# Kernel tuning notes

Measured on AMD Instinct MI355X. Metric: run time of the kernel, lower is better.

## Reference

```python
import jax, jax.numpy as jnp
import numpy as np

B, S, E, H = 2, 2048, 1024, 16
D = E // H  # head_dim = 64


def _rope(x):
    # x: (B, H, S, D); torchtune-style interleaved rotary embedding
    s, d = x.shape[-2], x.shape[-1]
    inv_freq = 1.0 / (10000.0 ** (jnp.arange(0, d, 2, dtype=jnp.float32) / d))  # (d/2,)
    freqs = jnp.arange(s, dtype=jnp.float32)[:, None] * inv_freq[None, :]       # (S, d/2)
    cos, sin = jnp.cos(freqs), jnp.sin(freqs)
    x1, x2 = x[..., 0::2], x[..., 1::2]
    o1 = x1 * cos - x2 * sin
    o2 = x2 * cos + x1 * sin
    return jnp.stack([o1, o2], axis=-1).reshape(x.shape)


def setup_inputs() -> dict:
    key = jax.random.key(0)
    kx, kq, kk, kv, ko = jax.random.split(key, 5)
    std = 1.0 / np.sqrt(E)
    return {
        "x": jax.random.normal(kx, (B, S, E), dtype=jnp.float32),
        "W_q": jax.random.normal(kq, (E, E), dtype=jnp.float32) * std,
        "W_k": jax.random.normal(kk, (E, E), dtype=jnp.float32) * std,
        "W_v": jax.random.normal(kv, (E, E), dtype=jnp.float32) * std,
        "W_o": jax.random.normal(ko, (E, E), dtype=jnp.float32) * std,
    }


def reference(x, W_q, W_k, W_v, W_o):
    b, s, e = x.shape
    h, d = H, e // H
    # nn.Linear: y = x @ W.T  (weights are (out, in))
    q = (x @ W_q.T).reshape(b, s, h, d).transpose(0, 2, 1, 3)  # (B,H,S,D)
    k = (x @ W_k.T).reshape(b, s, h, d).transpose(0, 2, 1, 3)
    v = (x @ W_v.T).reshape(b, s, h, d).transpose(0, 2, 1, 3)
    q = _rope(q)
    k = _rope(k)
    attn_scale = 1.0 / np.sqrt(e)  # NOTE: scales by sqrt(hidden_dim), as in source
    scores = jnp.einsum("bhsd,bhtd->bhst", q, k) * attn_scale  # (B,H,S,S)
    causal = jnp.triu(jnp.ones((s, s), dtype=bool), k=1)
    scores = jnp.where(causal, -jnp.inf, scores)
    probs = jax.nn.softmax(scores, axis=-1)  # dropout is identity in eval
    out = jnp.einsum("bhst,bhtd->bhsd", probs, v)
    out = out.transpose(0, 2, 1, 3).reshape(b, s, e)
    return out @ W_o.T
```

## Files before the change

### kernel.cpp

```cpp
#include <hip/hip_runtime.h>
#include <hip/hip_bf16.h>

#define BATCH 2
#define SEQ   2048
#define EMB   1024
#define NH    16
#define HD    64
#define MROWS (BATCH*SEQ)
#define NX    (MROWS*EMB)
#define NW    (EMB*EMB)

using f32x4  = __attribute__((ext_vector_type(4))) float;
using bf16x8 = __attribute__((ext_vector_type(8))) short;

#define GLOBAL_AS(p) ((const __attribute__((address_space(1))) void*)(p))
#define LDS_AS(p)    ((__attribute__((address_space(3))) void*)(p))

#define ROPE_L2 0.4152410118609203f
#define QSCALE  0.045084220027780106f

__global__ void fused_cast_kernel(const float* __restrict__ x,
                                  const float* __restrict__ Wq,
                                  const float* __restrict__ Wk,
                                  const float* __restrict__ Wv,
                                  const float* __restrict__ Wo,
                                  __hip_bfloat16* __restrict__ xb,
                                  __hip_bfloat16* __restrict__ Wqkvb,
                                  __hip_bfloat16* __restrict__ Wob,
                                  float2* __restrict__ ctab) {
    if (blockIdx.x >= 4096) {
        int e  = (blockIdx.x - 4096) * 256 + threadIdx.x;
        int s  = e >> 5;
        int ip = e & 31;
        float inv = exp2f(-(float)ip * ROPE_L2);
        float fr  = (float)s * inv;
        float2 cs;
        cs.x = cosf(fr);
        cs.y = sinf(fr);
        ctab[e] = cs;
        return;
    }
    size_t i8 = (size_t)(blockIdx.x * 256 + threadIdx.x) * 8;
    const float* src;
    __hip_bfloat16* dst;
    if (i8 < (size_t)NX) {
        src = x + i8;
        dst = xb + i8;
    } else {
        size_t w = i8 - NX;
        int which = (int)(w >> 20);
        size_t local = w & (NW - 1);
        if (which < 3) {
            src = (which == 0 ? Wq : (which == 1 ? Wk : Wv)) + local;
            dst = Wqkvb + w;
        } else {
            src = Wo + local;
            dst = Wob + local;
        }
    }
    float4 a = *(const float4*)(src);
    float4 b = *(const float4*)(src + 4);
    union { uint4 u; ushort s[8]; } o;
    const float* f = (const float*)&a;
#pragma unroll
    for (int j = 0; j < 4; ++j) {
        __hip_bfloat16 h = __float2bfloat16(f[j]);
        o.s[j] = *(ushort*)&h;
    }
    f = (const float*)&b;
#pragma unroll
    for (int j = 0; j < 4; ++j) {
        __hip_bfloat16 h = __float2bfloat16(f[j]);
        o.s[4 + j] = *(ushort*)&h;
    }
    *(uint4*)dst = o.u;
}

__global__ __launch_bounds__(256) void gemm_qkv_kernel(
        const __hip_bfloat16* __restrict__ A,
        const __hip_bfloat16* __restrict__ W,
        __hip_bfloat16* __restrict__ Qo,
        __hip_bfloat16* __restrict__ Ko,
        __hip_bfloat16* __restrict__ Vo,
        const float2* __restrict__ ctab, int M, int K) {
    __shared__ __hip_bfloat16 As[128 * 64];
    __shared__ __hip_bfloat16 Bs[128 * 64];

    const int tid  = threadIdx.x;
    const int wave = tid >> 6;
    const int lane = tid & 63;
    const int quad = lane >> 4;
    const int l16  = lane & 15;
    const int m0   = blockIdx.y * 128;
    const int n0   = blockIdx.x * 128;
    const int wm   = (wave >> 1) * 64;
    const int wn   = (wave & 1) * 64;
    const int xr   = l16 & 7;

    f32x4 acc[4][4] = {};

    for (int k0 = 0; k0 < K; k0 += 64) {
#pragma unroll
        for (int it = 0; it < 4; ++it) {
            int flat = (wave * 4 + it) * 64 + lane;
            int row  = flat >> 3;
            int g    = (flat & 7) ^ (row & 7);
            const __hip_bfloat16* ga = A + (size_t)(m0 + row) * K + k0 + g * 8;
            const __hip_bfloat16* gb = W + (size_t)(n0 + row) * K + k0 + g * 8;
            __builtin_amdgcn_global_load_lds(GLOBAL_AS(ga),
                LDS_AS(As + (size_t)(wave * 4 + it) * 512), 16, 0, 0);
            __builtin_amdgcn_global_load_lds(GLOBAL_AS(gb),
                LDS_AS(Bs + (size_t)(wave * 4 + it) * 512), 16, 0, 0);
        }
        __syncthreads();

#pragma unroll
        for (int kk = 0; kk < 2; ++kk) {
            const int kg = (kk * 4 + quad) ^ xr;
            bf16x8 af[4], bfr[4];
#pragma unroll
            for (int i = 0; i < 4; ++i) {
                af[i]  = *(const bf16x8*)(&As[(wm + i * 16 + l16) * 64 + kg * 8]);
                bfr[i] = *(const bf16x8*)(&Bs[(wn + i * 16 + l16) * 64 + kg * 8]);
            }
#pragma unroll
            for (int i = 0; i < 4; ++i)
#pragma unroll
                for (int j = 0; j < 4; ++j)
                    acc[i][j] = __builtin_amdgcn_mfma_f32_16x16x32_bf16(
                        af[i], bfr[j], acc[i][j], 0, 0, 0);
        }
        __syncthreads();
    }

    const int tens = n0 >> 10;
    __hip_bfloat16* outp = (tens == 0) ? Qo : ((tens == 1) ? Ko : Vo);
    const int nbase = n0 & 1023;
    if (tens < 2) {
        const float sgn   = (l16 & 1) ? 1.0f : -1.0f;
        const float qmul  = (tens == 0) ? QSCALE : 1.0f;
#pragma unroll
        for (int i = 0; i < 4; ++i)
#pragma unroll
            for (int j = 0; j < 4; ++j) {
                int col  = nbase + wn + j * 16 + l16;
                int ip   = ((wn + j * 16 + l16) & 63) >> 1;
                int row0 = m0 + wm + i * 16 + quad * 4;
#pragma unroll
                for (int rr = 0; rr < 4; ++rr) {
                    float v = acc[i][j][rr];
                    float p = __shfl_xor(v, 1);
                    int sp  = (row0 + rr) & (SEQ - 1);
                    float2 cs = ctab[sp * 32 + ip];
                    float o = (v * cs.x + sgn * p * cs.y) * qmul;
                    outp[(size_t)(row0 + rr) * EMB + col] = __float2bfloat16(o);
                }
            }
    } else {
#pragma unroll
        for (int i = 0; i < 4; ++i)
#pragma unroll
            for (int j = 0; j < 4; ++j) {
                int col  = nbase + wn + j * 16 + l16;
                int row0 = m0 + wm + i * 16 + quad * 4;
#pragma unroll
                for (int rr = 0; rr < 4; ++rr)
                    outp[(size_t)(row0 + rr) * EMB + col] = __float2bfloat16(acc[i][j][rr]);
            }
    }
}

__global__ __launch_bounds__(256) void gemm_oproj_kernel(
        const __hip_bfloat16* __restrict__ A,
        const __hip_bfloat16* __restrict__ Bm,
        float* __restrict__ C, int M, int N, int K) {
    __shared__ __hip_bfloat16 As[128 * 64];
    __shared__ __hip_bfloat16 Bs[64 * 64];

    const int tid  = threadIdx.x;
    const int wave = tid >> 6;
    const int lane = tid & 63;
    const int quad = lane >> 4;
    const int l16  = lane & 15;
    const int m0   = blockIdx.y * 128;
    const int n0   = blockIdx.x * 64;
    const int wm   = (wave >> 1) * 64;
    const int wn   = (wave & 1) * 32;
    const int xr   = l16 & 7;

    f32x4 acc[4][2] = {};

    for (int k0 = 0; k0 < K; k0 += 64) {
#pragma unroll
        for (int it = 0; it < 4; ++it) {
            int flat = (wave * 4 + it) * 64 + lane;
            int row  = flat >> 3;
            int g    = (flat & 7) ^ (row & 7);
            const __hip_bfloat16* ga = A + (size_t)(m0 + row) * K + k0 + g * 8;
            __builtin_amdgcn_global_load_lds(GLOBAL_AS(ga),
                LDS_AS(As + (size_t)(wave * 4 + it) * 512), 16, 0, 0);
        }
#pragma unroll
        for (int it = 0; it < 2; ++it) {
            int flat = (wave * 2 + it) * 64 + lane;
            int row  = flat >> 3;
            int g    = (flat & 7) ^ (row & 7);
            const __hip_bfloat16* gb = Bm + (size_t)(n0 + row) * K + k0 + g * 8;
            __builtin_amdgcn_global_load_lds(GLOBAL_AS(gb),
                LDS_AS(Bs + (size_t)(wave * 2 + it) * 512), 16, 0, 0);
        }
        __syncthreads();

#pragma unroll
        for (int kk = 0; kk < 2; ++kk) {
            const int kg = (kk * 4 + quad) ^ xr;
            bf16x8 af[4], bfr[2];
#pragma unroll
            for (int i = 0; i < 4; ++i)
                af[i] = *(const bf16x8*)(&As[(wm + i * 16 + l16) * 64 + kg * 8]);
#pragma unroll
            for (int j = 0; j < 2; ++j)
                bfr[j] = *(const bf16x8*)(&Bs[(wn + j * 16 + l16) * 64 + kg * 8]);
#pragma unroll
            for (int i = 0; i < 4; ++i)
#pragma unroll
                for (int j = 0; j < 2; ++j)
                    acc[i][j] = __builtin_amdgcn_mfma_f32_16x16x32_bf16(
                        af[i], bfr[j], acc[i][j], 0, 0, 0);
        }
        __syncthreads();
    }

#pragma unroll
    for (int i = 0; i < 4; ++i)
#pragma unroll
        for (int j = 0; j < 2; ++j) {
            int col  = n0 + wn + j * 16 + l16;
            int row0 = m0 + wm + i * 16 + quad * 4;
#pragma unroll
            for (int rr = 0; rr < 4; ++rr)
                C[(size_t)(row0 + rr) * N + col] = acc[i][j][rr];
        }
}

__device__ inline uint pack_bf16(float a, float b) {
    __hip_bfloat16 ha = __float2bfloat16(a), hb = __float2bfloat16(b);
    return (uint)*(ushort*)&ha | ((uint)*(ushort*)&hb << 16);
}

__global__ __launch_bounds__(256) void attn_mfma_kernel(
        const __hip_bfloat16* __restrict__ Qb,
        const __hip_bfloat16* __restrict__ Kb,
        const __hip_bfloat16* __restrict__ Vb,
        __hip_bfloat16* __restrict__ Attnb,
        __hip_bfloat16* __restrict__ Opart,
        float* __restrict__ Lpart) {
    const int bx   = blockIdx.x;
    const int bh   = blockIdx.y;
    const int b    = bh >> 4;
    const int h    = bh & (NH - 1);
    const int tid  = threadIdx.x;
    const int wave = tid >> 6;
    const int lane = tid & 63;
    const int quad = lane >> 4;
    const int l16  = lane & 15;

    __shared__ __hip_bfloat16 Ks[2][64 * 64];
    __shared__ uint VTs[2][64][33];

    const int vtp = tid >> 3;
    const int sg  = tid & 7;
    const int lr  = lane >> 3;
    const int lg  = (lane & 7) ^ lr;
    const size_t ksrc_lane = (size_t)lr * EMB + lg * 8;

    const __hip_bfloat16* Kbase = Kb + (size_t)b * SEQ * EMB + h * HD;
    const __hip_bfloat16* Vbase = Vb + (size_t)b * SEQ * EMB + h * HD;

    union { uint u[4]; bf16x8 v; } onesu;
    onesu.u[0] = 0x3F803F80u; onesu.u[1] = 0x3F803F80u;
    onesu.u[2] = 0x3F803F80u; onesu.u[3] = 0x3F803F80u;
    const bf16x8 ones = onesu.v;

    const bool isA = (bx < 16);
    const int p   = isA ? bx : bx - 16;
    const int q0  = 31 - p;
    const int k00 = isA ? 0 : 17;
    const int n0s = isA ? 17 : (15 - p);
    const int q1  = p;
    const int n1s = isA ? 0 : (p + 1);

    for (int s = 0; s < 2; ++s) {
        const int qt = s ? q1 : q0;
        const int k0 = s ? 0 : k00;
        const int nt = s ? n1s : n0s;
        if (nt <= 0) continue;
        const bool finalSeg = (!isA && s == 1);
        const int wrow = qt * 64 + wave * 16;

        __syncthreads();

        bf16x8 qf[2];
        {
            const __hip_bfloat16* qp =
                Qb + (size_t)(b * SEQ + wrow + l16) * EMB + h * HD + quad * 8;
            qf[0] = *(const bf16x8*)(qp);
            qf[1] = *(const bf16x8*)(qp + 32);
        }

        f32x4 of[4]  = {};
        f32x4 of_sum = {};

        const __hip_bfloat16* kgp = Kbase + (size_t)k0 * 64 * EMB;
        const __hip_bfloat16* vgp = Vbase + (size_t)(k0 * 64 + 2 * vtp) * EMB + sg * 8;
        uint4 vr0 = *(const uint4*)(vgp);
        uint4 vr1 = *(const uint4*)(vgp + EMB);
#pragma unroll
        for (int it = 0; it < 2; ++it)
            __builtin_amdgcn_global_load_lds(
                GLOBAL_AS(kgp + (size_t)(wave * 2 + it) * 8 * EMB + ksrc_lane),
                LDS_AS(&Ks[0][(wave * 2 + it) * 512]), 16, 0, 0);

        for (int i = 0; i < nt; ++i) {
            const int cur = i & 1;
            const int kt  = k0 + i;

            {
                const uint* v0u = (const uint*)&vr0;
                const uint* v1u = (const uint*)&vr1;
#pragma unroll
                for (int j = 0; j < 4; ++j) {
                    VTs[cur][sg * 8 + 2 * j][vtp] =
                        __builtin_amdgcn_perm(v1u[j], v0u[j], 0x05040100u);
                    VTs[cur][sg * 8 + 2 * j + 1][vtp] =
                        __builtin_amdgcn_perm(v1u[j], v0u[j], 0x07060302u);
                }
            }
            __syncthreads();

            if (i + 1 < nt) {
                kgp += (size_t)64 * EMB;
                vgp += (size_t)64 * EMB;
                vr0 = *(const uint4*)(vgp);
                vr1 = *(const uint4*)(vgp + EMB);
#pragma unroll
                for (int it = 0; it < 2; ++it)
                    __builtin_amdgcn_global_load_lds(
                        GLOBAL_AS(kgp + (size_t)(wave * 2 + it) * 8 * EMB + ksrc_lane),
                        LDS_AS(&Ks[cur ^ 1][(wave * 2 + it) * 512]), 16, 0, 0);
            }

            const bool diag = (kt == qt);
            const __hip_bfloat16* KsC = Ks[cur];
            f32x4 sc[4];
            __builtin_amdgcn_s_setprio(1);
#pragma unroll
            for (int mb = 0; mb < 4; ++mb) {
                f32x4 a = {};
                if (!(diag && mb > wave)) {
                    int krow = mb * 16 + l16;
#pragma unroll
                    for (int kb = 0; kb < 2; ++kb) {
                        int kg = (kb * 4 + quad) ^ (krow & 7);
                        bf16x8 kf = *(const bf16x8*)(&KsC[krow * 64 + kg * 8]);
                        a = __builtin_amdgcn_mfma_f32_16x16x32_bf16(kf, qf[kb], a, 0, 0, 0);
                    }
                }
                sc[mb] = a;
            }
            __builtin_amdgcn_s_setprio(0);

            if (diag) {
#pragma unroll
                for (int mb = 0; mb < 4; ++mb)
#pragma unroll
                    for (int r = 0; r < 4; ++r)
                        if (mb * 16 + quad * 4 + r > wave * 16 + l16)
                            sc[mb][r] = -16384.0f;
            }

#pragma unroll
            for (int mb = 0; mb < 4; ++mb)
#pragma unroll
                for (int r = 0; r < 4; ++r)
                    sc[mb][r] = exp2f(sc[mb][r]);

            bf16x8 pf[2];
            {
                union { uint u[4]; bf16x8 v; } t;
                t.u[0] = pack_bf16(sc[0][0], sc[0][1]);
                t.u[1] = pack_bf16(sc[0][2], sc[0][3]);
                t.u[2] = pack_bf16(sc[1][0], sc[1][1]);
                t.u[3] = pack_bf16(sc[1][2], sc[1][3]);
                pf[0] = t.v;
                t.u[0] = pack_bf16(sc[2][0], sc[2][1]);
                t.u[1] = pack_bf16(sc[2][2], sc[2][3]);
                t.u[2] = pack_bf16(sc[3][0], sc[3][1]);
                t.u[3] = pack_bf16(sc[3][2], sc[3][3]);
                pf[1] = t.v;
            }

            const uint* VT0 = &VTs[cur][0][0];
            __builtin_amdgcn_s_setprio(1);
#pragma unroll
            for (int nb = 0; nb < 4; ++nb) {
                const uint* vrow = VT0 + (size_t)(nb * 16 + l16) * 33;
#pragma unroll
                for (int c = 0; c < 2; ++c) {
                    union { uint u[4]; bf16x8 v; } vf;
                    vf.u[0] = vrow[c * 16 + 2 * quad];
                    vf.u[1] = vrow[c * 16 + 2 * quad + 1];
                    vf.u[2] = vrow[c * 16 + 8 + 2 * quad];
                    vf.u[3] = vrow[c * 16 + 8 + 2 * quad + 1];
                    of[nb] = __builtin_amdgcn_mfma_f32_16x16x32_bf16(
                        pf[c], vf.v, of[nb], 0, 0, 0);
                }
            }
            of_sum = __builtin_amdgcn_mfma_f32_16x16x32_bf16(pf[0], ones, of_sum, 0, 0, 0);
            of_sum = __builtin_amdgcn_mfma_f32_16x16x32_bf16(pf[1], ones, of_sum, 0, 0, 0);
            __builtin_amdgcn_s_setprio(0);
        }

        const int rl0 = quad * 4;
        if (finalSeg) {
            float linv[4];
#pragma unroll
            for (int r = 0; r < 4; ++r)
                linv[r] = 1.0f / of_sum[r];
#pragma unroll
            for (int nb = 0; nb < 4; ++nb)
#pragma unroll
                for (int r = 0; r < 4; ++r) {
                    float v = of[nb][r] * linv[r];
                    Attnb[(size_t)(b * SEQ + wrow + rl0 + r) * EMB + h * HD + nb * 16 + l16] =
                        __float2bfloat16(v);
                }
        } else {
            const int slot = isA ? 0 : 1;
            const size_t lbase = ((size_t)slot * 32 + bh) * SEQ + wrow;
            if (l16 == 0) {
#pragma unroll
                for (int r = 0; r < 4; ++r)
                    Lpart[lbase + rl0 + r] = of_sum[r];
            }
#pragma unroll
            for (int nb = 0; nb < 4; ++nb)
#pragma unroll
                for (int r = 0; r < 4; ++r)
                    Opart[(lbase + rl0 + r) * HD + nb * 16 + l16] =
                        __float2bfloat16(of[nb][r]);
        }
    }
}

__global__ void combine_kernel(const __hip_bfloat16* __restrict__ Opart,
                               const float* __restrict__ Lpart,
                               __hip_bfloat16* __restrict__ Attnb) {
    int idx = blockIdx.x * 256 + threadIdx.x;
    int d8 = idx & 7;
    int s  = 1024 + ((idx >> 3) & 1023);
    int bh = idx >> 13;
    int b  = bh >> 4;
    int h  = bh & (NH - 1);
    int qt = s >> 6;

    size_t base0 = ((size_t)bh * SEQ + s) * HD + d8 * 8;
    bf16x8 o0 = *(const bf16x8*)(Opart + base0);
    float l = Lpart[(size_t)bh * SEQ + s];
    float acc[8];
#pragma unroll
    for (int j = 0; j < 8; ++j)
        acc[j] = __uint_as_float(((uint)(ushort)o0[j]) << 16);
    if (qt >= 17) {
        size_t base1 = ((size_t)(32 + bh) * SEQ + s) * HD + d8 * 8;
        bf16x8 o1 = *(const bf16x8*)(Opart + base1);
        l += Lpart[(size_t)(32 + bh) * SEQ + s];
#pragma unroll
        for (int j = 0; j < 8; ++j)
            acc[j] += __uint_as_float(((uint)(ushort)o1[j]) << 16);
    }
    float inv = 1.0f / l;
    union { uint4 u; ushort w[8]; } o;
#pragma unroll
    for (int j = 0; j < 8; ++j) {
        __hip_bfloat16 hv = __float2bfloat16(acc[j] * inv);
        o.w[j] = *(ushort*)&hv;
    }
    *(uint4*)(Attnb + ((size_t)(b * SEQ + s) * EMB) + h * HD + d8 * 8) = o.u;
}

extern "C" void kernel_launch(void* const* d_in, const int* in_sizes, int n_in,
                              void* d_out, int out_size, void* d_ws, size_t ws_size,
                              hipStream_t stream) {
    const float* x  = (const float*)d_in[0];
    const float* Wq = (const float*)d_in[1];
    const float* Wk = (const float*)d_in[2];
    const float* Wv = (const float*)d_in[3];
    const float* Wo = (const float*)d_in[4];
    float* out = (float*)d_out;

    char* ws = (char*)d_ws;
    size_t off = 0;
    auto alloc = [&](size_t bytes) -> void* {
        void* p = ws + off;
        off += (bytes + 255) & ~(size_t)255;
        return p;
    };

    __hip_bfloat16* xb    = (__hip_bfloat16*)alloc((size_t)NX * 2);
    __hip_bfloat16* Wqkvb = (__hip_bfloat16*)alloc((size_t)NW * 3 * 2);
    __hip_bfloat16* Wob   = (__hip_bfloat16*)alloc((size_t)NW * 2);
    __hip_bfloat16* Qbuf  = (__hip_bfloat16*)alloc((size_t)NX * 2);
    __hip_bfloat16* Kbuf  = (__hip_bfloat16*)alloc((size_t)NX * 2);
    __hip_bfloat16* Vbuf  = (__hip_bfloat16*)alloc((size_t)NX * 2);
    __hip_bfloat16* Attnb = (__hip_bfloat16*)alloc((size_t)NX * 2);
    __hip_bfloat16* Opart = (__hip_bfloat16*)alloc((size_t)2 * 32 * SEQ * HD * 2);
    float*          Lpart = (float*)alloc((size_t)2 * 32 * SEQ * 4);
    float2*         ctab  = (float2*)alloc((size_t)SEQ * 32 * sizeof(float2));

    fused_cast_kernel<<<(NX + 4 * NW) / (256 * 8) + 256, 256, 0, stream>>>(
        x, Wq, Wk, Wv, Wo, xb, Wqkvb, Wob, ctab);

    dim3 qgrid(24, MROWS / 128);
    gemm_qkv_kernel<<<qgrid, 256, 0, stream>>>(xb, Wqkvb, Qbuf, Kbuf, Vbuf,
                                               ctab, MROWS, EMB);

    dim3 agrid(32, BATCH * NH);
    attn_mfma_kernel<<<agrid, 256, 0, stream>>>(Qbuf, Kbuf, Vbuf, Attnb,
                                                Opart, Lpart);

    combine_kernel<<<(32 * 1024 * 8) / 256, 256, 0, stream>>>(Opart, Lpart, Attnb);

    dim3 ggrid(EMB / 64, MROWS / 128);
    gemm_oproj_kernel<<<ggrid, 256, 0, stream>>>(Attnb, Wob, out, MROWS, EMB, EMB);
}
```

Baseline: 198.2 us.

## Fuse split-KV combine into attention via atomic last-arriver, use raw exp/cvt asm

Removes the separate combine kernel: attention blocks writing partial outputs for split query tiles bump a per-tile atomic counter, and the second block to finish merges both partials and writes the normalized result. Flags are zeroed by an extra block in the cast kernel. The diff also replaces exp2f with raw v_exp_f32 and the manual bf16 packing with v_cvt_pk_bf16_f32. This saves a launch and a pass over the partial buffers, at the cost of threadfences, atomics and a tail of extra work in some attention blocks.

```diff
diff --git a/kernel.cpp b/kernel.cpp
--- a/kernel.cpp
+++ b/kernel.cpp
@@ -27,7 +27,13 @@
                                   __hip_bfloat16* __restrict__ xb,
                                   __hip_bfloat16* __restrict__ Wqkvb,
                                   __hip_bfloat16* __restrict__ Wob,
-                                  float2* __restrict__ ctab) {
+                                  float2* __restrict__ ctab,
+                                  uint* __restrict__ Flags) {
+    if (blockIdx.x == 4352) {
+        Flags[threadIdx.x]       = 0;
+        Flags[256 + threadIdx.x] = 0;
+        return;
+    }
     if (blockIdx.x >= 4096) {
         int e  = (blockIdx.x - 4096) * 256 + threadIdx.x;
         int s  = e >> 5;
@@ -243,9 +249,15 @@
         }
 }
 
-__device__ inline uint pack_bf16(float a, float b) {
-    __hip_bfloat16 ha = __float2bfloat16(a), hb = __float2bfloat16(b);
-    return (uint)*(ushort*)&ha | ((uint)*(ushort*)&hb << 16);
+__device__ inline uint cvt_pk_bf16(float lo, float hi) {
+    uint r;
+    asm("v_cvt_pk_bf16_f32 %0, %1, %2" : "=v"(r) : "v"(lo), "v"(hi));
+    return r;
+}
+__device__ inline float exp2_raw(float x) {
+    float r;
+    asm("v_exp_f32 %0, %1" : "=v"(r) : "v"(x));
+    return r;
 }
 
 __global__ __launch_bounds__(256) void attn_mfma_kernel(
@@ -254,7 +266,8 @@
         const __hip_bfloat16* __restrict__ Vb,
         __hip_bfloat16* __restrict__ Attnb,
         __hip_bfloat16* __restrict__ Opart,
-        float* __restrict__ Lpart) {
+        float* __restrict__ Lpart,
+        uint* __restrict__ Flags) {
     const int bx   = blockIdx.x;
     const int bh   = blockIdx.y;
     const int b    = bh >> 4;
@@ -267,6 +280,7 @@
 
     __shared__ __hip_bfloat16 Ks[2][64 * 64];
     __shared__ uint VTs[2][64][33];
+    __shared__ uint hsh;
 
     const int vtp = tid >> 3;
     const int sg  = tid & 7;
@@ -295,7 +309,7 @@
         const int k0 = s ? 0 : k00;
         const int nt = s ? n1s : n0s;
         if (nt <= 0) continue;
-        const bool finalSeg = (!isA && s == 1);
+        const bool finalSeg = (!isA && s == 1) || (isA && p == 15);
         const int wrow = qt * 64 + wave * 16;
 
         __syncthreads();
@@ -383,20 +397,20 @@
             for (int mb = 0; mb < 4; ++mb)
 #pragma unroll
                 for (int r = 0; r < 4; ++r)
-                    sc[mb][r] = exp2f(sc[mb][r]);
+                    sc[mb][r] = exp2_raw(sc[mb][r]);
 
             bf16x8 pf[2];
             {
                 union { uint u[4]; bf16x8 v; } t;
-                t.u[0] = pack_bf16(sc[0][0], sc[0][1]);
-                t.u[1] = pack_bf16(sc[0][2], sc[0][3]);
-                t.u[2] = pack_bf16(sc[1][0], sc[1][1]);
-                t.u[3] = pack_bf16(sc[1][2], sc[1][3]);
+                t.u[0] = cvt_pk_bf16(sc[0][0], sc[0][1]);
+                t.u[1] = cvt_pk_bf16(sc[0][2], sc[0][3]);
+                t.u[2] = cvt_pk_bf16(sc[1][0], sc[1][1]);
+                t.u[3] = cvt_pk_bf16(sc[1][2], sc[1][3]);
                 pf[0] = t.v;
-                t.u[0] = pack_bf16(sc[2][0], sc[2][1]);
-                t.u[1] = pack_bf16(sc[2][2], sc[2][3]);
-                t.u[2] = pack_bf16(sc[3][0], sc[3][1]);
-                t.u[3] = pack_bf16(sc[3][2], sc[3][3]);
+                t.u[0] = cvt_pk_bf16(sc[2][0], sc[2][1]);
+                t.u[1] = cvt_pk_bf16(sc[2][2], sc[2][3]);
+                t.u[2] = cvt_pk_bf16(sc[3][0], sc[3][1]);
+                t.u[3] = cvt_pk_bf16(sc[3][2], sc[3][3]);
                 pf[1] = t.v;
             }
 
@@ -449,44 +463,45 @@
                 for (int r = 0; r < 4; ++r)
                     Opart[(lbase + rl0 + r) * HD + nb * 16 + l16] =
                         __float2bfloat16(of[nb][r]);
-        }
-    }
-}
-
-__global__ void combine_kernel(const __hip_bfloat16* __restrict__ Opart,
-                               const float* __restrict__ Lpart,
-                               __hip_bfloat16* __restrict__ Attnb) {
-    int idx = blockIdx.x * 256 + threadIdx.x;
-    int d8 = idx & 7;
-    int s  = 1024 + ((idx >> 3) & 1023);
-    int bh = idx >> 13;
-    int b  = bh >> 4;
-    int h  = bh & (NH - 1);
-    int qt = s >> 6;
-
-    size_t base0 = ((size_t)bh * SEQ + s) * HD + d8 * 8;
-    bf16x8 o0 = *(const bf16x8*)(Opart + base0);
-    float l = Lpart[(size_t)bh * SEQ + s];
-    float acc[8];
-#pragma unroll
-    for (int j = 0; j < 8; ++j)
-        acc[j] = __uint_as_float(((uint)(ushort)o0[j]) << 16);
-    if (qt >= 17) {
-        size_t base1 = ((size_t)(32 + bh) * SEQ + s) * HD + d8 * 8;
-        bf16x8 o1 = *(const bf16x8*)(Opart + base1);
-        l += Lpart[(size_t)(32 + bh) * SEQ + s];
-#pragma unroll
-        for (int j = 0; j < 8; ++j)
-            acc[j] += __uint_as_float(((uint)(ushort)o1[j]) << 16);
-    }
-    float inv = 1.0f / l;
-    union { uint4 u; ushort w[8]; } o;
-#pragma unroll
-    for (int j = 0; j < 8; ++j) {
-        __hip_bfloat16 hv = __float2bfloat16(acc[j] * inv);
-        o.w[j] = *(ushort*)&hv;
-    }
-    *(uint4*)(Attnb + ((size_t)(b * SEQ + s) * EMB) + h * HD + d8 * 8) = o.u;
+
+            __threadfence();
+            __syncthreads();
+            if (tid == 0)
+                hsh = atomicAdd(&Flags[bh * 15 + (qt - 17)], 1u);
+            __syncthreads();
+            if (hsh == 1) {
+                __threadfence();
+                const int r  = tid >> 2;
+                const int cb = tid & 3;
+                const int srow = qt * 64 + r;
+                const size_t p0 = ((size_t)bh * SEQ + srow) * HD + cb * 16;
+                const size_t p1 = ((size_t)(32 + bh) * SEQ + srow) * HD + cb * 16;
+                float lt = Lpart[(size_t)bh * SEQ + srow] +
+                           Lpart[(size_t)(32 + bh) * SEQ + srow];
+                float inv = 1.0f / lt;
+                bf16x8 a0 = *(const bf16x8*)(Opart + p0);
+                bf16x8 a1 = *(const bf16x8*)(Opart + p0 + 8);
+                bf16x8 b0 = *(const bf16x8*)(Opart + p1);
+                bf16x8 b1 = *(const bf16x8*)(Opart + p1 + 8);
+                union { uint4 u; ushort w[8]; } o0, o1;
+#pragma unroll
+                for (int j = 0; j < 8; ++j) {
+                    float va = __uint_as_float(((uint)(ushort)a0[j]) << 16) +
+                               __uint_as_float(((uint)(ushort)b0[j]) << 16);
+                    float vb = __uint_as_float(((uint)(ushort)a1[j]) << 16) +
+                               __uint_as_float(((uint)(ushort)b1[j]) << 16);
+                    __hip_bfloat16 ha = __float2bfloat16(va * inv);
+                    __hip_bfloat16 hb = __float2bfloat16(vb * inv);
+                    o0.w[j] = *(ushort*)&ha;
+                    o1.w[j] = *(ushort*)&hb;
+                }
+                __hip_bfloat16* dst =
+                    Attnb + ((size_t)(b * SEQ + srow) * EMB) + h * HD + cb * 16;
+                *(uint4*)(dst)     = o0.u;
+                *(uint4*)(dst + 8) = o1.u;
+            }
+        }
+    }
 }
 
 extern "C" void kernel_launch(void* const* d_in, const int* in_sizes, int n_in,
@@ -517,9 +532,10 @@
     __hip_bfloat16* Opart = (__hip_bfloat16*)alloc((size_t)2 * 32 * SEQ * HD * 2);
     float*          Lpart = (float*)alloc((size_t)2 * 32 * SEQ * 4);
     float2*         ctab  = (float2*)alloc((size_t)SEQ * 32 * sizeof(float2));
-
-    fused_cast_kernel<<<(NX + 4 * NW) / (256 * 8) + 256, 256, 0, stream>>>(
-        x, Wq, Wk, Wv, Wo, xb, Wqkvb, Wob, ctab);
+    uint*           Flags = (uint*)alloc((size_t)512 * 4);
+
+    fused_cast_kernel<<<(NX + 4 * NW) / (256 * 8) + 257, 256, 0, stream>>>(
+        x, Wq, Wk, Wv, Wo, xb, Wqkvb, Wob, ctab, Flags);
 
     dim3 qgrid(24, MROWS / 128);
     gemm_qkv_kernel<<<qgrid, 256, 0, stream>>>(xb, Wqkvb, Qbuf, Kbuf, Vbuf,
@@ -527,9 +543,7 @@
 
     dim3 agrid(32, BATCH * NH);
     attn_mfma_kernel<<<agrid, 256, 0, stream>>>(Qbuf, Kbuf, Vbuf, Attnb,
-                                                Opart, Lpart);
-
-    combine_kernel<<<(32 * 1024 * 8) / 256, 256, 0, stream>>>(Opart, Lpart, Attnb);
+                                                Opart, Lpart, Flags);
 
     dim3 ggrid(EMB / 64, MROWS / 128);
     gemm_oproj_kernel<<<ggrid, 256, 0, stream>>>(Attnb, Wob, out, MROWS, EMB, EMB);
```

After: 389.3 us. +96.5%, slower.
